# Optimization experiments

Measured on AMD Instinct MI355X. Metric: run time of the kernel, lower is better.

Reference implementation:

```python
import jax, jax.numpy as jnp
import numpy as np
from jax import lax

N = 400000
INC = 128
MIDC = 64
OUTC = 128
KVOL = 27
EPS = 1e-5


def _bn(h, g, b, m, v):
    return (h - m) * (g * lax.rsqrt(v + EPS)) + b


def setup_inputs() -> dict:
    key = jax.random.key(0)
    ks = jax.random.split(key, 16)
    x = jax.random.normal(ks[0], (N, INC), jnp.float32)
    nb = jax.random.randint(ks[1], (KVOL, N), 0, N, jnp.int32)
    s1 = 1.0 / np.sqrt(INC)
    s2 = 1.0 / np.sqrt(MIDC * KVOL)
    s3 = 1.0 / np.sqrt(MIDC)
    w1 = jax.random.normal(ks[2], (INC, MIDC), jnp.float32) * s1
    w2 = jax.random.normal(ks[3], (KVOL, MIDC, MIDC), jnp.float32) * s2
    w3 = jax.random.normal(ks[4], (MIDC, OUTC), jnp.float32) * s3
    def bn_params(k, c):
        k1, k2, k3, k4 = jax.random.split(k, 4)
        return (jax.random.normal(k1, (c,), jnp.float32) * 0.1 + 1.0,
                jax.random.normal(k2, (c,), jnp.float32) * 0.1,
                jax.random.normal(k3, (c,), jnp.float32) * 0.1,
                jax.random.uniform(k4, (c,), jnp.float32) + 0.5)
    bn1_g, bn1_b, bn1_m, bn1_v = bn_params(ks[5], MIDC)
    bn2_g, bn2_b, bn2_m, bn2_v = bn_params(ks[6], MIDC)
    bn3_g, bn3_b, bn3_m, bn3_v = bn_params(ks[7], OUTC)
    return dict(x=x, nb=nb, w1=w1, w2=w2, w3=w3,
                bn1_g=bn1_g, bn1_b=bn1_b, bn1_m=bn1_m, bn1_v=bn1_v,
                bn2_g=bn2_g, bn2_b=bn2_b, bn2_m=bn2_m, bn2_v=bn2_v,
                bn3_g=bn3_g, bn3_b=bn3_b, bn3_m=bn3_m, bn3_v=bn3_v)


def reference(x, nb, w1, w2, w3,
              bn1_g, bn1_b, bn1_m, bn1_v,
              bn2_g, bn2_b, bn2_m, bn2_v,
              bn3_g, bn3_b, bn3_m, bn3_v):
    # 1x1 sparse conv == pointwise matmul
    h = jax.nn.relu(_bn(x @ w1, bn1_g, bn1_b, bn1_m, bn1_v))  # [N, midc]

    # ks=3 sparse conv: gather-matmul-accumulate over 27 kernel offsets
    def body(acc, kw):
        idx, wk = kw  # idx: [N] gather indices, wk: [midc, midc]
        return acc + h[idx] @ wk, None
    acc0 = jnp.zeros((N, MIDC), h.dtype)
    h2, _ = lax.scan(body, acc0, (nb, w2))
    h2 = jax.nn.relu(_bn(h2, bn2_g, bn2_b, bn2_m, bn2_v))

    # 1x1 conv + BN, then residual add (identity downsample: inc==outc, stride==1)
    h3 = _bn(h2 @ w3, bn3_g, bn3_b, bn3_m, bn3_v)  # [N, outc]
    return jax.nn.relu(h3 + x)
```

## Files before the change

### kernel.cpp

```cpp
#include <hip/hip_runtime.h>

#define N_PTS 400000
#define EPS 1e-5f

typedef __attribute__((ext_vector_type(8))) short short8;
typedef __attribute__((ext_vector_type(4))) float f32x4;

constexpr size_t H_OFF   = 0;
constexpr size_t H2_OFF  = 51200000;
constexpr size_t W1T_OFF = 102400000;
constexpr size_t W2S_OFF = W1T_OFF + 16384;
constexpr size_t W3T_OFF = W2S_OFF + 221184;
constexpr size_t BNC_OFF = W3T_OFF + 16384;

__device__ __forceinline__ short f2bf(float f) {
  unsigned u = __builtin_bit_cast(unsigned, f);
  u += 0x7FFFu + ((u >> 16) & 1u);
  return (short)(u >> 16);
}

__global__ __launch_bounds__(256) void prep_kernel(
    const float* __restrict__ w1, const float* __restrict__ w2,
    const float* __restrict__ w3,
    const float* __restrict__ g1, const float* __restrict__ b1,
    const float* __restrict__ m1, const float* __restrict__ v1,
    const float* __restrict__ g2, const float* __restrict__ b2,
    const float* __restrict__ m2, const float* __restrict__ v2,
    const float* __restrict__ g3, const float* __restrict__ b3,
    const float* __restrict__ m3, const float* __restrict__ v3,
    short* __restrict__ w1t, short* __restrict__ w2s,
    short* __restrict__ w3t, float* __restrict__ bnc) {
  int tid = blockIdx.x * 256 + threadIdx.x;
  int gs = gridDim.x * 256;
  for (int i = tid; i < 128 * 64; i += gs) {
    int k = i >> 6, n = i & 63;
    w1t[n * 128 + k] = f2bf(w1[i]);
  }
  for (int i = tid; i < 27 * 64 * 64; i += gs) {
    int kk = i >> 12, r = i & 4095, k = r >> 6, n = r & 63;
    int byte = (n * 64 + k) * 2;
    byte ^= (n & 7) << 4;
    w2s[kk * 4096 + (byte >> 1)] = f2bf(w2[i]);
  }
  for (int i = tid; i < 64 * 128; i += gs) {
    int k = i >> 7, n = i & 127;
    w3t[n * 64 + k] = f2bf(w3[i]);
  }
  if (tid < 64) {
    float s = g1[tid] * rsqrtf(v1[tid] + EPS);
    bnc[tid] = s; bnc[64 + tid] = b1[tid] - m1[tid] * s;
  } else if (tid < 128) {
    int c = tid - 64;
    float s = g2[c] * rsqrtf(v2[c] + EPS);
    bnc[128 + c] = s; bnc[192 + c] = b2[c] - m2[c] * s;
  } else if (tid < 256) {
    int c = tid - 128;
    float s = g3[c] * rsqrtf(v3[c] + EPS);
    bnc[256 + c] = s; bnc[384 + c] = b3[c] - m3[c] * s;
  }
}

__global__ __launch_bounds__(256) void stage1_kernel(
    const float* __restrict__ x, const short* __restrict__ w1t,
    const float* __restrict__ bnc, short* __restrict__ h) {
  const int lane = threadIdx.x & 63;
  const int wid = threadIdx.x >> 6;
  const int lr = lane & 15, lk = lane >> 4;
  const long wbase = ((long)blockIdx.x * 4 + wid) * 64;
  if (wbase >= N_PTS) return;

  short8 bf[4][4];
#pragma unroll
  for (int nf = 0; nf < 4; ++nf)
#pragma unroll
    for (int ks = 0; ks < 4; ++ks)
      bf[nf][ks] = *(const short8*)(w1t + (nf * 16 + lr) * 128 + ks * 32 + lk * 8);

  float s[4], t[4];
#pragma unroll
  for (int nf = 0; nf < 4; ++nf) {
    int ch = nf * 16 + lr;
    s[nf] = bnc[ch]; t[nf] = bnc[64 + ch];
  }

#pragma unroll
  for (int mt = 0; mt < 4; ++mt) {
    f32x4 acc[4];
#pragma unroll
    for (int nf = 0; nf < 4; ++nf) acc[nf] = f32x4{0.f, 0.f, 0.f, 0.f};
    const float* xr = x + (wbase + mt * 16 + lr) * 128 + lk * 8;
#pragma unroll
    for (int ks = 0; ks < 4; ++ks) {
      f32x4 lo = *(const f32x4*)(xr + ks * 32);
      f32x4 hi = *(const f32x4*)(xr + ks * 32 + 4);
      short8 a;
#pragma unroll
      for (int j = 0; j < 4; ++j) { a[j] = f2bf(lo[j]); a[4 + j] = f2bf(hi[j]); }
#pragma unroll
      for (int nf = 0; nf < 4; ++nf)
        acc[nf] = __builtin_amdgcn_mfma_f32_16x16x32_bf16(a, bf[nf][ks], acc[nf], 0, 0, 0);
    }
    short* hr = h + (wbase + mt * 16) * 64;
#pragma unroll
    for (int nf = 0; nf < 4; ++nf) {
      int ch = nf * 16 + lr;
#pragma unroll
      for (int j = 0; j < 4; ++j) {
        int row = lk * 4 + j;
        float v = acc[nf][j] * s[nf] + t[nf];
        v = v > 0.f ? v : 0.f;
        hr[row * 64 + ch] = f2bf(v);
      }
    }
  }
}

__global__ __launch_bounds__(256, 4) void stage2_kernel(
    const short* __restrict__ h, const int* __restrict__ nb,
    const short* __restrict__ w2s, const float* __restrict__ bnc,
    short* __restrict__ h2) {
  __shared__ __align__(16) short bbuf[2][4096];
  const int tid = threadIdx.x;
  const int lane = tid & 63;
  const int wid = tid >> 6;
  const int lr = lane & 15, lk = lane >> 4;
  const long wbase = ((long)blockIdx.x * 4 + wid) * 32;

  int boff[4][2];
#pragma unroll
  for (int nf = 0; nf < 4; ++nf) {
    int row = nf * 16 + lr;
#pragma unroll
    for (int ks = 0; ks < 2; ++ks)
      boff[nf][ks] = ((row * 128 + ks * 64 + lk * 16) ^ ((row & 7) << 4)) >> 1;
  }

  f32x4 acc[2][4];
#pragma unroll
  for (int mt = 0; mt < 2; ++mt)
#pragma unroll
    for (int nf = 0; nf < 4; ++nf) acc[mt][nf] = f32x4{0.f, 0.f, 0.f, 0.f};

  const int* nb0 = nb + wbase + lr;

  int idxq[4][2];
  short8 acur[2][2], anext[2][2];

#pragma unroll
  for (int kk = 0; kk < 3; ++kk)
#pragma unroll
    for (int mt = 0; mt < 2; ++mt)
      idxq[kk][mt] = nb0[(long)kk * N_PTS + mt * 16];

#pragma unroll
  for (int mt = 0; mt < 2; ++mt)
#pragma unroll
    for (int ks = 0; ks < 2; ++ks)
      acur[mt][ks] = *(const short8*)(h + (long)idxq[0][mt] * 64 + ks * 32 + lk * 8);

  {
    short8 b0a = *(const short8*)(w2s + tid * 16);
    short8 b0b = *(const short8*)(w2s + tid * 16 + 8);
    short8 b1a = *(const short8*)(w2s + 4096 + tid * 16);
    short8 b1b = *(const short8*)(w2s + 4096 + tid * 16 + 8);
    *(short8*)(&bbuf[0][tid * 16]) = b0a;
    *(short8*)(&bbuf[0][tid * 16 + 8]) = b0b;
    *(short8*)(&bbuf[1][tid * 16]) = b1a;
    *(short8*)(&bbuf[1][tid * 16 + 8]) = b1b;
  }
  asm volatile("s_waitcnt lgkmcnt(0)" ::: "memory");
  __builtin_amdgcn_s_barrier();

#pragma unroll
  for (int k = 0; k < 27; ++k) {
    const int kp = k & 1;
    short8 bsa, bsb;
    if (k + 2 < 27) {
      bsa = *(const short8*)(w2s + (k + 2) * 4096 + tid * 16);
      bsb = *(const short8*)(w2s + (k + 2) * 4096 + tid * 16 + 8);
    }
    if (k + 3 < 27) {
#pragma unroll
      for (int mt = 0; mt < 2; ++mt)
        idxq[(k + 3) & 3][mt] = nb0[(long)(k + 3) * N_PTS + mt * 16];
    }
    if (k + 1 < 27) {
#pragma unroll
      for (int mt = 0; mt < 2; ++mt)
#pragma unroll
        for (int ks = 0; ks < 2; ++ks)
          anext[mt][ks] = *(const short8*)(h + (long)idxq[(k + 1) & 3][mt] * 64 + ks * 32 + lk * 8);
    }
#pragma unroll
    for (int nf = 0; nf < 4; ++nf) {
#pragma unroll
      for (int ks = 0; ks < 2; ++ks) {
        short8 bf = *(const short8*)(&bbuf[kp][boff[nf][ks]]);
#pragma unroll
        for (int mt = 0; mt < 2; ++mt)
          acc[mt][nf] = __builtin_amdgcn_mfma_f32_16x16x32_bf16(acur[mt][ks], bf, acc[mt][nf], 0, 0, 0);
      }
    }
    asm volatile("s_waitcnt lgkmcnt(0)" ::: "memory");
    __builtin_amdgcn_s_barrier();
    if (k + 2 < 27) {
      *(short8*)(&bbuf[kp][tid * 16]) = bsa;
      *(short8*)(&bbuf[kp][tid * 16 + 8]) = bsb;
    }
    if (k + 1 < 27) {
#pragma unroll
      for (int mt = 0; mt < 2; ++mt)
#pragma unroll
        for (int ks = 0; ks < 2; ++ks)
          acur[mt][ks] = anext[mt][ks];
    }
  }

  float s2[4], t2[4];
#pragma unroll
  for (int nf = 0; nf < 4; ++nf) {
    int ch = nf * 16 + lr;
    s2[nf] = bnc[128 + ch]; t2[nf] = bnc[192 + ch];
  }

#pragma unroll
  for (int mt = 0; mt < 2; ++mt) {
    short* h2r = h2 + (wbase + mt * 16) * 64;
#pragma unroll
    for (int nf = 0; nf < 4; ++nf) {
      int ch = nf * 16 + lr;
#pragma unroll
      for (int j = 0; j < 4; ++j) {
        float v = acc[mt][nf][j] * s2[nf] + t2[nf];
        v = v > 0.f ? v : 0.f;
        h2r[(lk * 4 + j) * 64 + ch] = f2bf(v);
      }
    }
  }
}

__global__ __launch_bounds__(256) void stage3_kernel(
    const short* __restrict__ h2, const short* __restrict__ w3t,
    const float* __restrict__ bnc, const float* __restrict__ x,
    float* __restrict__ out) {
  const int lane = threadIdx.x & 63;
  const int wid = threadIdx.x >> 6;
  const int lr = lane & 15, lk = lane >> 4;
  const long wbase = ((long)blockIdx.x * 4 + wid) * 64;
  if (wbase >= N_PTS) return;

  short8 b3[8][2];
#pragma unroll
  for (int nf = 0; nf < 8; ++nf)
#pragma unroll
    for (int ks = 0; ks < 2; ++ks)
      b3[nf][ks] = *(const short8*)(w3t + (nf * 16 + lr) * 64 + ks * 32 + lk * 8);

#pragma unroll
  for (int mt = 0; mt < 4; ++mt) {
    short8 a3[2];
#pragma unroll
    for (int ks = 0; ks < 2; ++ks)
      a3[ks] = *(const short8*)(h2 + (wbase + mt * 16 + lr) * 64 + ks * 32 + lk * 8);

    f32x4 acc3[8];
#pragma unroll
    for (int nf = 0; nf < 8; ++nf) acc3[nf] = f32x4{0.f, 0.f, 0.f, 0.f};
#pragma unroll
    for (int ks = 0; ks < 2; ++ks)
#pragma unroll
      for (int nf = 0; nf < 8; ++nf)
        acc3[nf] = __builtin_amdgcn_mfma_f32_16x16x32_bf16(a3[ks], b3[nf][ks], acc3[nf], 0, 0, 0);

    const float* xr = x + (wbase + mt * 16 + lk * 4) * 128;
    float* outr = out + (wbase + mt * 16 + lk * 4) * 128;
#pragma unroll
    for (int nf = 0; nf < 8; ++nf) {
      int ch = nf * 16 + lr;
      float s3 = bnc[256 + ch], t3 = bnc[384 + ch];
#pragma unroll
      for (int j = 0; j < 4; ++j) {
        float v = acc3[nf][j] * s3 + t3 + xr[j * 128 + ch];
        outr[j * 128 + ch] = v > 0.f ? v : 0.f;
      }
    }
  }
}

extern "C" void kernel_launch(void* const* d_in, const int* in_sizes, int n_in,
                              void* d_out, int out_size, void* d_ws, size_t ws_size,
                              hipStream_t stream) {
  const float* x  = (const float*)d_in[0];
  const int*   nb = (const int*)d_in[1];
  const float* w1 = (const float*)d_in[2];
  const float* w2 = (const float*)d_in[3];
  const float* w3 = (const float*)d_in[4];
  const float* g1 = (const float*)d_in[5];
  const float* b1 = (const float*)d_in[6];
  const float* m1 = (const float*)d_in[7];
  const float* v1 = (const float*)d_in[8];
  const float* g2 = (const float*)d_in[9];
  const float* b2 = (const float*)d_in[10];
  const float* m2 = (const float*)d_in[11];
  const float* v2 = (const float*)d_in[12];
  const float* g3 = (const float*)d_in[13];
  const float* b3 = (const float*)d_in[14];
  const float* m3 = (const float*)d_in[15];
  const float* v3 = (const float*)d_in[16];

  char* ws = (char*)d_ws;
  short* hbuf  = (short*)(ws + H_OFF);
  short* h2buf = (short*)(ws + H2_OFF);
  short* w1t   = (short*)(ws + W1T_OFF);
  short* w2s   = (short*)(ws + W2S_OFF);
  short* w3t   = (short*)(ws + W3T_OFF);
  float* bnc   = (float*)(ws + BNC_OFF);
  float* outp  = (float*)d_out;

  prep_kernel<<<128, 256, 0, stream>>>(w1, w2, w3,
                                       g1, b1, m1, v1,
                                       g2, b2, m2, v2,
                                       g3, b3, m3, v3,
                                       w1t, w2s, w3t, bnc);
  stage1_kernel<<<1563, 256, 0, stream>>>(x, w1t, bnc, hbuf);
  stage2_kernel<<<3125, 256, 0, stream>>>(hbuf, nb, w2s, bnc, h2buf);
  stage3_kernel<<<1563, 256, 0, stream>>>(h2buf, w3t, bnc, x, outp);
}
```

Baseline: 389.6 us.

## Shrink stage2 wave tile to 16 rows and deepen gather prefetch pipeline

Stage2 now gives each wave 16 points instead of 32 and launches twice as many blocks. The freed registers pay for a deeper software pipeline: neighbor indices are fetched four offsets ahead, gathered rows two offsets ahead through a three-slot ring, and weight slices three ahead. A sched_barrier keeps these loads issued before the MFMAs. The aim is to hide random-gather latency with more loads in flight, but each block now repeats the shared-memory weight staging and barriers for half as much MFMA work, and the occupancy hint drops from 4 to 3.

```diff
diff --git a/kernel.cpp b/kernel.cpp
--- a/kernel.cpp
+++ b/kernel.cpp
@@ -115,7 +115,7 @@
   }
 }
 
-__global__ __launch_bounds__(256, 4) void stage2_kernel(
+__global__ __launch_bounds__(256, 3) void stage2_kernel(
     const short* __restrict__ h, const int* __restrict__ nb,
     const short* __restrict__ w2s, const float* __restrict__ bnc,
     short* __restrict__ h2) {
@@ -124,7 +124,7 @@
   const int lane = tid & 63;
   const int wid = tid >> 6;
   const int lr = lane & 15, lk = lane >> 4;
-  const long wbase = ((long)blockIdx.x * 4 + wid) * 32;
+  const long wbase = ((long)blockIdx.x * 4 + wid) * 16;
 
   int boff[4][2];
 #pragma unroll
@@ -135,84 +135,69 @@
       boff[nf][ks] = ((row * 128 + ks * 64 + lk * 16) ^ ((row & 7) << 4)) >> 1;
   }
 
-  f32x4 acc[2][4];
-#pragma unroll
-  for (int mt = 0; mt < 2; ++mt)
-#pragma unroll
-    for (int nf = 0; nf < 4; ++nf) acc[mt][nf] = f32x4{0.f, 0.f, 0.f, 0.f};
+  f32x4 acc[4];
+#pragma unroll
+  for (int nf = 0; nf < 4; ++nf) acc[nf] = f32x4{0.f, 0.f, 0.f, 0.f};
 
   const int* nb0 = nb + wbase + lr;
 
-  int idxq[4][2];
-  short8 acur[2][2], anext[2][2];
-
-#pragma unroll
-  for (int kk = 0; kk < 3; ++kk)
-#pragma unroll
-    for (int mt = 0; mt < 2; ++mt)
-      idxq[kk][mt] = nb0[(long)kk * N_PTS + mt * 16];
-
-#pragma unroll
-  for (int mt = 0; mt < 2; ++mt)
-#pragma unroll
-    for (int ks = 0; ks < 2; ++ks)
-      acur[mt][ks] = *(const short8*)(h + (long)idxq[0][mt] * 64 + ks * 32 + lk * 8);
+  int idxq[4];
+  short8 ag[3][2];
+  short8 bsq[2][2];
+
+#pragma unroll
+  for (int kk = 0; kk < 4; ++kk)
+    idxq[kk] = nb0[(long)kk * N_PTS];
 
   {
     short8 b0a = *(const short8*)(w2s + tid * 16);
     short8 b0b = *(const short8*)(w2s + tid * 16 + 8);
     short8 b1a = *(const short8*)(w2s + 4096 + tid * 16);
     short8 b1b = *(const short8*)(w2s + 4096 + tid * 16 + 8);
+    bsq[0][0] = *(const short8*)(w2s + 2 * 4096 + tid * 16);
+    bsq[0][1] = *(const short8*)(w2s + 2 * 4096 + tid * 16 + 8);
     *(short8*)(&bbuf[0][tid * 16]) = b0a;
     *(short8*)(&bbuf[0][tid * 16 + 8]) = b0b;
     *(short8*)(&bbuf[1][tid * 16]) = b1a;
     *(short8*)(&bbuf[1][tid * 16 + 8]) = b1b;
   }
+#pragma unroll
+  for (int kk = 0; kk < 2; ++kk)
+#pragma unroll
+    for (int ks = 0; ks < 2; ++ks)
+      ag[kk][ks] = *(const short8*)(h + (long)idxq[kk] * 64 + ks * 32 + lk * 8);
+
   asm volatile("s_waitcnt lgkmcnt(0)" ::: "memory");
   __builtin_amdgcn_s_barrier();
 
 #pragma unroll
   for (int k = 0; k < 27; ++k) {
-    const int kp = k & 1;
-    short8 bsa, bsb;
+    if (k + 3 < 27) {
+      bsq[(k + 3) & 1][0] = *(const short8*)(w2s + (k + 3) * 4096 + tid * 16);
+      bsq[(k + 3) & 1][1] = *(const short8*)(w2s + (k + 3) * 4096 + tid * 16 + 8);
+    }
+    if (k + 4 < 27) {
+      idxq[(k + 4) & 3] = nb0[(long)(k + 4) * N_PTS];
+    }
     if (k + 2 < 27) {
-      bsa = *(const short8*)(w2s + (k + 2) * 4096 + tid * 16);
-      bsb = *(const short8*)(w2s + (k + 2) * 4096 + tid * 16 + 8);
-    }
-    if (k + 3 < 27) {
-#pragma unroll
-      for (int mt = 0; mt < 2; ++mt)
-        idxq[(k + 3) & 3][mt] = nb0[(long)(k + 3) * N_PTS + mt * 16];
-    }
-    if (k + 1 < 27) {
-#pragma unroll
-      for (int mt = 0; mt < 2; ++mt)
-#pragma unroll
-        for (int ks = 0; ks < 2; ++ks)
-          anext[mt][ks] = *(const short8*)(h + (long)idxq[(k + 1) & 3][mt] * 64 + ks * 32 + lk * 8);
-    }
+#pragma unroll
+      for (int ks = 0; ks < 2; ++ks)
+        ag[(k + 2) % 3][ks] = *(const short8*)(h + (long)idxq[(k + 2) & 3] * 64 + ks * 32 + lk * 8);
+    }
+    __builtin_amdgcn_sched_barrier(0);
 #pragma unroll
     for (int nf = 0; nf < 4; ++nf) {
 #pragma unroll
       for (int ks = 0; ks < 2; ++ks) {
-        short8 bf = *(const short8*)(&bbuf[kp][boff[nf][ks]]);
-#pragma unroll
-        for (int mt = 0; mt < 2; ++mt)
-          acc[mt][nf] = __builtin_amdgcn_mfma_f32_16x16x32_bf16(acur[mt][ks], bf, acc[mt][nf], 0, 0, 0);
+        short8 bf = *(const short8*)(&bbuf[k & 1][boff[nf][ks]]);
+        acc[nf] = __builtin_amdgcn_mfma_f32_16x16x32_bf16(ag[k % 3][ks], bf, acc[nf], 0, 0, 0);
       }
     }
     asm volatile("s_waitcnt lgkmcnt(0)" ::: "memory");
     __builtin_amdgcn_s_barrier();
     if (k + 2 < 27) {
-      *(short8*)(&bbuf[kp][tid * 16]) = bsa;
-      *(short8*)(&bbuf[kp][tid * 16 + 8]) = bsb;
-    }
-    if (k + 1 < 27) {
-#pragma unroll
-      for (int mt = 0; mt < 2; ++mt)
-#pragma unroll
-        for (int ks = 0; ks < 2; ++ks)
-          acur[mt][ks] = anext[mt][ks];
+      *(short8*)(&bbuf[k & 1][tid * 16]) = bsq[k & 1][0];
+      *(short8*)(&bbuf[k & 1][tid * 16 + 8]) = bsq[k & 1][1];
     }
   }
 
@@ -223,18 +208,15 @@
     s2[nf] = bnc[128 + ch]; t2[nf] = bnc[192 + ch];
   }
 
-#pragma unroll
-  for (int mt = 0; mt < 2; ++mt) {
-    short* h2r = h2 + (wbase + mt * 16) * 64;
-#pragma unroll
-    for (int nf = 0; nf < 4; ++nf) {
-      int ch = nf * 16 + lr;
-#pragma unroll
-      for (int j = 0; j < 4; ++j) {
-        float v = acc[mt][nf][j] * s2[nf] + t2[nf];
-        v = v > 0.f ? v : 0.f;
-        h2r[(lk * 4 + j) * 64 + ch] = f2bf(v);
-      }
+  short* h2r = h2 + wbase * 64;
+#pragma unroll
+  for (int nf = 0; nf < 4; ++nf) {
+    int ch = nf * 16 + lr;
+#pragma unroll
+    for (int j = 0; j < 4; ++j) {
+      float v = acc[nf][j] * s2[nf] + t2[nf];
+      v = v > 0.f ? v : 0.f;
+      h2r[(lk * 4 + j) * 64 + ch] = f2bf(v);
     }
   }
 }
@@ -323,6 +305,6 @@
                                        g3, b3, m3, v3,
                                        w1t, w2s, w3t, bnc);
   stage1_kernel<<<1563, 256, 0, stream>>>(x, w1t, bnc, hbuf);
-  stage2_kernel<<<3125, 256, 0, stream>>>(hbuf, nb, w2s, bnc, h2buf);
+  stage2_kernel<<<6250, 256, 0, stream>>>(hbuf, nb, w2s, bnc, h2buf);
   stage3_kernel<<<1563, 256, 0, stream>>>(h2buf, w3t, bnc, x, outp);
 }
```

Measured after the change: 405.3 us. +4.0%, slower.
